# Performance work log

Hardware: AMD Instinct MI355X
Metric: run time of the kernel (lower is better)

Reference implementation:

```python
import jax, jax.numpy as jnp
import numpy as np

N = 100000   # nodes
E = 1600000  # edges (avg degree 16)
H = 128      # hidden_dim
G = 256      # graphs in batch
IN = 2       # input feature dim (GCNConv(2, hidden_dim))


def setup_inputs() -> dict:
    key = jax.random.key(0)
    ks = jax.random.split(key, 12)
    def lin(k, fan_in, shape):
        # kaiming-uniform-ish init, scale irrelevant for correctness testing
        return jax.random.uniform(k, shape, jnp.float32, -1.0, 1.0) / np.sqrt(fan_in).astype(np.float32)
    return {
        "x": jax.random.normal(ks[0], (N, IN), jnp.float32),
        "edge_src": jax.random.randint(ks[1], (E,), 0, N, jnp.int32),
        "edge_dst": jax.random.randint(ks[2], (E,), 0, N, jnp.int32),
        "batch_ids": jnp.sort(jax.random.randint(ks[3], (N,), 0, G, jnp.int32)),
        "num_graphs": G,
        "W1": lin(ks[4], IN, (IN, H)), "b1": jnp.zeros((H,), jnp.float32),
        "W2": lin(ks[5], H, (H, H)),  "b2": jnp.zeros((H,), jnp.float32),
        "fc1_W": lin(ks[6], H, (H, H)), "fc1_b": lin(ks[7], H, (H,)),
        "fc2_W": lin(ks[8], H, (H, 1)), "fc2_b": lin(ks[9], H, (1,)),
    }


def gcn_layer(x, W, b, src, dst, n):
    # PyG GCNConv: add self-loops, symmetric deg^{-1/2} normalization,
    # linear transform, scatter-add aggregation, bias.
    h = x @ W                                                     # [N, H]
    deg = jax.ops.segment_sum(jnp.ones_like(src, jnp.float32), dst, num_segments=n) + 1.0  # +1 self-loop
    dinv = jax.lax.rsqrt(deg)                                     # [N]
    norm = dinv[src] * dinv[dst]                                  # [E]
    agg = jax.ops.segment_sum(h[src] * norm[:, None], dst, num_segments=n)  # [N, H]
    # self-loop contribution: deg_i^{-1/2} * deg_i^{-1/2} = 1/deg_i
    return agg + h * (1.0 / deg)[:, None] + b


def reference(x, edge_src, edge_dst, batch_ids, num_graphs,
              W1, b1, W2, b2, fc1_W, fc1_b, fc2_W, fc2_b):
    n = x.shape[0]
    h = jax.nn.relu(gcn_layer(x, W1, b1, edge_src, edge_dst, n))
    h = jax.nn.relu(gcn_layer(h, W2, b2, edge_src, edge_dst, n))
    # global_mean_pool
    sums = jax.ops.segment_sum(h, batch_ids, num_segments=num_graphs)            # [G, H]
    cnt = jax.ops.segment_sum(jnp.ones((n,), jnp.float32), batch_ids, num_segments=num_graphs)
    pooled = sums / jnp.maximum(cnt, 1.0)[:, None]
    h = jax.nn.relu(pooled @ fc1_W + fc1_b)
    return h @ fc2_W + fc2_b                                                     # [G, 1]
```

## Files before the change

### kernel.cpp

```cpp
#include <hip/hip_runtime.h>
#include <stdint.h>

#define HD 128
#define BSH 8
#define BNODES 256
#define PER 8
#define SCAP 256
#define BINBLK 256

typedef float f32x4 __attribute__((ext_vector_type(4)));
typedef float f32x2 __attribute__((ext_vector_type(2)));
typedef short s16x8 __attribute__((ext_vector_type(8)));

static inline int idiv(int a, int b) { return (a + b - 1) / b; }

__device__ __forceinline__ unsigned short f2b(float f) {
  unsigned u = __float_as_uint(f);
  return (unsigned short)((u + 0x7fffu + ((u >> 16) & 1u)) >> 16);
}

__global__ void __launch_bounds__(256) k_bincount(const int* __restrict__ edst,
                                                  int* __restrict__ cntm,
                                                  int E, int NB, int chunk) {
  __shared__ int hist[512];
  int blk = blockIdx.x;
  for (int b = threadIdx.x; b < 512; b += 256) hist[b] = 0;
  __syncthreads();
  int s0 = blk * chunk, s1 = min(E, s0 + chunk);
  for (int k = s0 + threadIdx.x; k < s1; k += 256)
    atomicAdd(&hist[edst[k] >> BSH], 1);
  __syncthreads();
  for (int b = threadIdx.x; b < NB; b += 256)
    cntm[(size_t)b * BINBLK + blk] = hist[b];
}

__global__ void k_scan1(const int* __restrict__ cnt, int* __restrict__ part, int N) {
  __shared__ int sh[256];
  int t = threadIdx.x;
  int base = blockIdx.x * 1024 + t * 4;
  int s = 0;
#pragma unroll
  for (int u = 0; u < 4; ++u) { int idx = base + u; if (idx < N) s += cnt[idx]; }
  sh[t] = s; __syncthreads();
  for (int off = 128; off > 0; off >>= 1) { if (t < off) sh[t] += sh[t + off]; __syncthreads(); }
  if (t == 0) part[blockIdx.x] = sh[0];
}

__global__ void k_scan2(int* part, int nb) {
  __shared__ int sh[1024];
  int t = threadIdx.x;
  int v = (t < nb) ? part[t] : 0;
  sh[t] = v;
  __syncthreads();
  for (int off = 1; off < 1024; off <<= 1) {
    int add = (t >= off) ? sh[t - off] : 0;
    __syncthreads();
    sh[t] += add;
    __syncthreads();
  }
  if (t < nb) part[t] = sh[t] - v;
}

__global__ void k_scan3(const int* __restrict__ cnt, const int* __restrict__ part,
                        int* __restrict__ out, int N) {
  __shared__ int sa[256], sb[256];
  int t = threadIdx.x;
  int base = blockIdx.x * 1024 + t * 4;
  int v[4]; int s = 0;
#pragma unroll
  for (int u = 0; u < 4; ++u) { int idx = base + u; v[u] = (idx < N) ? cnt[idx] : 0; s += v[u]; }
  sa[t] = s; __syncthreads();
  int* cur = sa; int* nxt = sb;
  for (int off = 1; off < 256; off <<= 1) {
    int val = cur[t] + ((t >= off) ? cur[t - off] : 0);
    nxt[t] = val; __syncthreads();
    int* tmp = cur; cur = nxt; nxt = tmp;
  }
  int excl = cur[t] - s + part[blockIdx.x];
#pragma unroll
  for (int u = 0; u < 4; ++u) {
    int idx = base + u;
    if (idx < N) { out[idx] = excl; excl += v[u]; }
  }
}

__global__ void __launch_bounds__(256) k_binscatter(const int* __restrict__ esrc,
                                                    const int* __restrict__ edst,
                                                    const int* __restrict__ scanM,
                                                    unsigned* __restrict__ recs,
                                                    int E, int NB, int chunk) {
  __shared__ int cur[512];
  int blk = blockIdx.x;
  for (int b = threadIdx.x; b < NB; b += 256) cur[b] = scanM[(size_t)b * BINBLK + blk];
  __syncthreads();
  int s0 = blk * chunk, s1 = min(E, s0 + chunk);
  for (int k = s0 + threadIdx.x; k < s1; k += 256) {
    int d = edst[k], s = esrc[k];
    int b = d >> BSH;
    int pos = atomicAdd(&cur[b], 1);
    recs[pos] = ((unsigned)(d & (BNODES - 1)) << 23) | (unsigned)s;
  }
}

__global__ void __launch_bounds__(256) k_bucketsort(const unsigned* __restrict__ recs,
                                                    const int* __restrict__ scanM,
                                                    const float* __restrict__ x,
                                                    const int* __restrict__ bids,
                                                    unsigned* __restrict__ ssrc16,
                                                    int* __restrict__ row_start,
                                                    int* __restrict__ cnt,
                                                    float* __restrict__ dinv,
                                                    float2* __restrict__ xs,
                                                    int* __restrict__ gstart,
                                                    int NB, int N, int G, int E) {
  __shared__ int count[BNODES], excl[BNODES], cur[BNODES], psum[32];
  int b = blockIdx.x;
  int t = threadIdx.x;
  count[t] = 0;
  __syncthreads();
  int rs = scanM[(size_t)b * BINBLK];
  int re = (b == NB - 1) ? E : scanM[(size_t)(b + 1) * BINBLK];
  int base_p = rs + b * BNODES;
  for (int k = rs + t; k < re; k += 256) atomicAdd(&count[recs[k] >> 23], 1);
  __syncthreads();
  if (t < 32) {
    int s = 0;
#pragma unroll
    for (int u = 0; u < 8; ++u) s += (count[t * 8 + u] + 1) & ~1;
    psum[t] = s;
  }
  __syncthreads();
  if (t == 0) {
    int run = 0;
    for (int d = 0; d < 32; ++d) { int v = psum[d]; psum[d] = run; run += v; }
  }
  __syncthreads();
  if (t < 32) {
    int run = psum[t];
#pragma unroll
    for (int u = 0; u < 8; ++u) {
      excl[t * 8 + u] = run;
      run += (count[t * 8 + u] + 1) & ~1;
    }
  }
  __syncthreads();
  {
    int d = t;
    int i = b * BNODES + d;
    if (i < N) {
      cnt[i] = count[d];
      row_start[i] = base_p + excl[d];
      if (count[d] & 1)
        ssrc16[base_p + excl[d] + count[d]] = (unsigned)N << 4;
      float di = rsqrtf((float)(count[d] + 1));
      dinv[i] = di;
      float2 xv = *(const float2*)&x[2 * i];
      xs[i] = make_float2(di * xv.x, di * xv.y);
      int g = bids[i];
      if (i == 0)
        for (int gg = 0; gg <= g; ++gg) gstart[gg] = 0;
      int gn = (i == N - 1) ? G : bids[i + 1];
      for (int gg = g + 1; gg <= gn; ++gg) gstart[gg] = i + 1;
    }
    cur[d] = excl[d];
  }
  __syncthreads();
  for (int k = rs + t; k < re; k += 256) {
    unsigned r = recs[k];
    int dl = r >> 23;
    int pos = base_p + atomicAdd(&cur[dl], 1);
    ssrc16[pos] = (r & 0x007fffffu) << 4;
  }
}

__global__ void k_aggx2(const int* __restrict__ row_start, const int* __restrict__ cnt,
                        const unsigned* __restrict__ ssrc16, const float2* __restrict__ xs,
                        const float* __restrict__ dinv, float4* __restrict__ td, int N) {
  int i = blockIdx.x * 256 + threadIdx.x;
  if (i >= N) return;
  int rs = row_start[i], re = rs + cnt[i];
  float a0 = 0.f, a1 = 0.f, b0 = 0.f, b1 = 0.f;
  int k = rs;
  for (; k + 3 < re; k += 4) {
    unsigned v0 = ssrc16[k] >> 4, v1 = ssrc16[k + 1] >> 4;
    unsigned v2 = ssrc16[k + 2] >> 4, v3 = ssrc16[k + 3] >> 4;
    float2 p0 = xs[v0], p1 = xs[v1], p2 = xs[v2], p3 = xs[v3];
    a0 += p0.x + p1.x; a1 += p0.y + p1.y;
    b0 += p2.x + p3.x; b1 += p2.y + p3.y;
  }
  for (; k < re; ++k) {
    float2 p = xs[ssrc16[k] >> 4];
    a0 += p.x; a1 += p.y;
  }
  a0 += b0; a1 += b1;
  float2 self = xs[i];
  float di = dinv[i];
  td[i] = make_float4(di * (a0 + self.x), di * (a1 + self.y), di, 0.f);
}

__global__ void __launch_bounds__(256) k_aggh(
    const int* __restrict__ row_start, const int* __restrict__ cnt,
    const unsigned* __restrict__ ssrc16, const float4* __restrict__ td,
    const float* __restrict__ W1, const float* __restrict__ b1,
    unsigned* __restrict__ m_b, int N) {
  __shared__ float4 sbuf[4][SCAP];
  int wave = threadIdx.x >> 6;
  int lane = threadIdx.x & 63;
  int wid = blockIdx.x * 4 + wave;
  int i0 = wid * PER;
  if (i0 >= N) return;
  int nn = min(N - i0, PER);
  int hl = lane >> 5;
  int fq = (lane & 31) * 4;
  f32x4 w0 = *(const f32x4*)&W1[fq];
  f32x4 w1 = *(const f32x4*)&W1[HD + fq];
  f32x4 bb = *(const f32x4*)&b1[fq];
  int mydeg = (lane < nn) ? cnt[i0 + lane] : 0;
  int myrow = (lane < nn) ? row_start[i0 + lane] : 0;
  float4 mytd = (lane < nn) ? td[i0 + lane] : make_float4(0.f, 0.f, 0.f, 0.f);
  int mx = __float_as_int(mytd.x), my = __float_as_int(mytd.y), mz = __float_as_int(mytd.z);
  int rs0 = __builtin_amdgcn_readfirstlane(myrow);
  int last = nn - 1;
  int rsEnd = __builtin_amdgcn_readlane(myrow, last) +
              ((__builtin_amdgcn_readlane(mydeg, last) + 1) & ~1);
  int total = rsEnd - rs0;
  const char* tdc = (const char*)td;
  bool staged = (total <= SCAP);
  if (staged) {
#pragma unroll
    for (int w = 0; w < SCAP / 64; ++w) {
      int sl = w * 64 + lane;
      if (sl < total) {
        unsigned off = ssrc16[rs0 + sl];
        sbuf[wave][sl] = *(const float4*)(tdc + off);
      }
    }
  }
  int k = 0;
  const f32x4 zero4 = {0.f, 0.f, 0.f, 0.f};
#define EDGE_F(T, ACC) { \
    f32x4 h = f32x4{T.y, T.y, T.y, T.y} * w1 + bb; \
    h = f32x4{T.x, T.x, T.x, T.x} * w0 + h; \
    h = __builtin_elementwise_max(h, zero4); \
    ACC = f32x4{T.z, T.z, T.z, T.z} * h + ACC; }
  for (int node = 0; node < nn; ++node) {
    int deg = __builtin_amdgcn_readlane(mydeg, node);
    int np = (deg + 1) >> 1;
    f32x4 acc = zero4, acc2 = zero4;
    if (staged) {
      const float4* buf = &sbuf[wave][k + hl];
      int p = 0;
      for (; p + 1 < np; p += 2) {
        float4 t0 = buf[2 * p];
        float4 t1 = buf[2 * p + 2];
        EDGE_F(t0, acc)
        EDGE_F(t1, acc2)
      }
      if (p < np) {
        float4 t0 = buf[2 * p];
        EDGE_F(t0, acc)
      }
    } else {
      for (int p = 0; p < np; ++p) {
        unsigned off = ssrc16[rs0 + k + 2 * p + hl];
        float4 t = *(const float4*)(tdc + off);
        EDGE_F(t, acc)
      }
    }
    k += np * 2;
#pragma unroll
    for (int c = 0; c < 4; ++c) acc[c] += acc2[c];
    f32x4 tot;
#pragma unroll
    for (int c = 0; c < 4; ++c) tot[c] = acc[c] + __shfl_xor(acc[c], 32);
    float tx = __int_as_float(__builtin_amdgcn_readlane(mx, node));
    float ty = __int_as_float(__builtin_amdgcn_readlane(my, node));
    float tz = __int_as_float(__builtin_amdgcn_readlane(mz, node));
    f32x4 h = f32x4{ty, ty, ty, ty} * w1 + bb;
    h = f32x4{tx, tx, tx, tx} * w0 + h;
    h = __builtin_elementwise_max(h, zero4);
    f32x4 r = f32x4{tz, tz, tz, tz} * h + tot;
    float v0 = (hl ? r[2] : r[0]) * tz;
    float v1 = (hl ? r[3] : r[1]) * tz;
    int j = hl ? (2 * (lane - 32) + 1) : (2 * lane);
    m_b[(unsigned)(i0 + node) * 64 + j] = ((unsigned)f2b(v1) << 16) | f2b(v0);
  }
#undef EDGE_F
}

__global__ void k_w2t(const float* __restrict__ W2, unsigned* __restrict__ w2f,
                      float4* __restrict__ td, int N) {
  int f = blockIdx.x * 256 + threadIdx.x;
  if (f == 0) td[N] = make_float4(0.f, 0.f, 0.f, 0.f);
  if (f >= 2048) return;
  int c = f >> 8, s = (f >> 6) & 3, lane = f & 63;
  int col = c * 16 + (lane & 15);
  int kb = s * 32 + (lane >> 4) * 8;
  unsigned hi4[4], lo4[4];
#pragma unroll
  for (int j = 0; j < 4; ++j) {
    float w0 = W2[(kb + 2 * j) * HD + col];
    float w1 = W2[(kb + 2 * j + 1) * HD + col];
    unsigned short h0 = f2b(w0), h1 = f2b(w1);
    float r0 = w0 - __uint_as_float((unsigned)h0 << 16);
    float r1 = w1 - __uint_as_float((unsigned)h1 << 16);
    unsigned short l0 = f2b(r0), l1 = f2b(r1);
    hi4[j] = ((unsigned)h1 << 16) | h0;
    lo4[j] = ((unsigned)l1 << 16) | l0;
  }
  *(uint4*)&w2f[f * 4] = make_uint4(hi4[0], hi4[1], hi4[2], hi4[3]);
  *(uint4*)&w2f[8192 + f * 4] = make_uint4(lo4[0], lo4[1], lo4[2], lo4[3]);
}

__global__ void __launch_bounds__(256) k_t2pool(
    const unsigned* __restrict__ m_b, const unsigned* __restrict__ w2f,
    const float* __restrict__ b2, const int* __restrict__ gstart,
    const float* __restrict__ fc1W, const float* __restrict__ fc1b,
    const float* __restrict__ fc2W, const float* __restrict__ fc2b,
    float* __restrict__ out, int N, int G) {
  __shared__ unsigned W[16384];
  __shared__ float pool[16][HD];
  __shared__ float ps[HD];
  __shared__ float rsh[HD];
  int g = blockIdx.x;
  for (int u = threadIdx.x; u < 4096; u += 256)
    *(uint4*)&W[u * 4] = *(const uint4*)&w2f[u * 4];
  for (int u = threadIdx.x; u < 16 * HD; u += 256) ((float*)pool)[u] = 0.f;
  const int lane = threadIdx.x & 63;
  const int wave = threadIdx.x >> 6;
  const int col = lane & 15;
  const int kg = lane >> 4;
  float bb[8];
#pragma unroll
  for (int c = 0; c < 8; ++c) bb[c] = b2[c * 16 + col];
  int s0 = gstart[g], e0 = gstart[g + 1];
  int ntiles = (e0 - s0 + 15) >> 4;
  float pacc[8];
#pragma unroll
  for (int c = 0; c < 8; ++c) pacc[c] = 0.f;
  __syncthreads();
  for (int tile = wave; tile < ntiles; tile += 4) {
    int rbase = s0 + tile * 16;
    int arow = rbase + col;
    if (arow >= N) arow = N - 1;
    f32x4 acc[8];
#pragma unroll
    for (int c = 0; c < 8; ++c) acc[c] = f32x4{0.f, 0.f, 0.f, 0.f};
#pragma unroll
    for (int s = 0; s < 4; ++s) {
      uint4 av = *(const uint4*)&m_b[((size_t)arow << 6) + s * 16 + kg * 4];
      s16x8 A = *(s16x8*)&av;
#pragma unroll
      for (int c = 0; c < 8; ++c) {
        int f = (c * 4 + s) * 64 + lane;
        s16x8 Bh = *(s16x8*)&W[f * 4];
        s16x8 Bl = *(s16x8*)&W[8192 + f * 4];
        acc[c] = __builtin_amdgcn_mfma_f32_16x16x32_bf16(A, Bh, acc[c], 0, 0, 0);
        acc[c] = __builtin_amdgcn_mfma_f32_16x16x32_bf16(A, Bl, acc[c], 0, 0, 0);
      }
    }
    int orow = rbase + kg * 4;
#pragma unroll
    for (int c = 0; c < 8; ++c) {
#pragma unroll
      for (int r = 0; r < 4; ++r) {
        if (orow + r < e0) pacc[c] += fmaxf(acc[c][r] + bb[c], 0.f);
      }
    }
  }
#pragma unroll
  for (int c = 0; c < 8; ++c) pool[wave * 4 + kg][c * 16 + col] = pacc[c];
  __syncthreads();
  int j = threadIdx.x;
  if (j < HD) {
    float a = 0.f;
#pragma unroll
    for (int r = 0; r < 16; ++r) a += pool[r][j];
    float cg = (float)(e0 - s0);
    cg = cg < 1.f ? 1.f : cg;
    ps[j] = a / cg;
  }
  __syncthreads();
  if (j < HD) {
    float a = fc1b[j];
#pragma unroll 4
    for (int k = 0; k < HD; ++k) a = fmaf(ps[k], fc1W[k * HD + j], a);
    rsh[j] = fmaxf(a, 0.f) * fc2W[j];
  }
  __syncthreads();
  for (int off = 64; off > 0; off >>= 1) {
    if (j < off) rsh[j] += rsh[j + off];
    __syncthreads();
  }
  if (j == 0) out[g] = rsh[0] + fc2b[0];
}

extern "C" void kernel_launch(void* const* d_in, const int* in_sizes, int n_in,
                              void* d_out, int out_size, void* d_ws, size_t ws_size,
                              hipStream_t stream) {
  const float* x    = (const float*)d_in[0];
  const int* esrc   = (const int*)d_in[1];
  const int* edst   = (const int*)d_in[2];
  const int* bids   = (const int*)d_in[3];
  const float* W1   = (const float*)d_in[5];
  const float* b1   = (const float*)d_in[6];
  const float* W2   = (const float*)d_in[7];
  const float* b2   = (const float*)d_in[8];
  const float* fc1W = (const float*)d_in[9];
  const float* fc1b = (const float*)d_in[10];
  const float* fc2W = (const float*)d_in[11];
  const float* fc2b = (const float*)d_in[12];
  float* out = (float*)d_out;

  const int N = in_sizes[0] / 2;
  const int E = in_sizes[1];
  const int G = out_size;

  const int NB = idiv(N, BNODES);
  const int M = NB * BINBLK;
  const int chunk = idiv(E, BINBLK);

  char* w = (char*)d_ws;
  size_t o = 0;
  auto take = [&](size_t b) -> char* {
    char* p = w + o;
    o = (o + b + 255) & ~(size_t)255;
    return p;
  };
  int*      cntm      = (int*)     take((size_t)M * 4);
  int*      scanM     = (int*)     take((size_t)M * 4);
  int*      part      = (int*)     take(4096);
  unsigned* recs      = (unsigned*)take((size_t)E * 4);
  unsigned* ssrc16    = (unsigned*)take((size_t)(E + N + 256) * 4);
  int*      cnt       = (int*)     take((size_t)N * 4);
  int*      row_start = (int*)     take((size_t)N * 4);
  float*    dinv      = (float*)   take((size_t)N * 4);
  float*    xs        = (float*)   take((size_t)N * 8);
  float*    td        = (float*)   take((size_t)(N + 1) * 16);
  int*      gstart    = (int*)     take((size_t)(G + 1) * 4);
  unsigned* m_b       = (unsigned*)take((size_t)N * 64 * 4);
  unsigned* w2f       = (unsigned*)take(16384 * 4);

  int nbM = idiv(M, 1024);
  k_w2t<<<8, 256, 0, stream>>>(W2, w2f, (float4*)td, N);
  k_bincount<<<BINBLK, 256, 0, stream>>>(edst, cntm, E, NB, chunk);
  k_scan1<<<nbM, 256, 0, stream>>>(cntm, part, M);
  k_scan2<<<1, 1024, 0, stream>>>(part, nbM);
  k_scan3<<<nbM, 256, 0, stream>>>(cntm, part, scanM, M);
  k_binscatter<<<BINBLK, 256, 0, stream>>>(esrc, edst, scanM, recs, E, NB, chunk);
  k_bucketsort<<<NB, 256, 0, stream>>>(recs, scanM, x, bids, ssrc16, row_start,
                                       cnt, dinv, (float2*)xs, gstart, NB, N, G, E);
  k_aggx2<<<idiv(N, 256), 256, 0, stream>>>(row_start, cnt, ssrc16, (const float2*)xs,
                                            dinv, (float4*)td, N);
  int waves = idiv(N, PER);
  k_aggh<<<idiv(waves, 4), 256, 0, stream>>>(row_start, cnt, ssrc16, (const float4*)td,
                                             W1, b1, m_b, N);
  k_t2pool<<<G, 256, 0, stream>>>(m_b, w2f, b2, gstart, fc1W, fc1b, fc2W, fc2b, out, N, G);
}
```

Before: 126.0 us.

## Stream edge gathers through double-buffered LDS batches and merge scan kernels

The layer-2 aggregation kernel no longer stages a whole wave's edges in a fixed 256-entry LDS buffer with a slow uncached fallback. It now walks edges in 64-entry batches, double-buffered, prefetching the next batch into registers while computing the current one, with a per-node state machine that spans batch boundaries. Nodes per wave go from 8 to 16. The three-kernel scan over the bin-count matrix becomes a single 1024-thread kernel, cutting two launches at the cost of running on one block.

```diff
diff --git a/kernel.cpp b/kernel.cpp
--- a/kernel.cpp
+++ b/kernel.cpp
@@ -4,8 +4,7 @@
 #define HD 128
 #define BSH 8
 #define BNODES 256
-#define PER 8
-#define SCAP 256
+#define PER 16
 #define BINBLK 256
 
 typedef float f32x4 __attribute__((ext_vector_type(4)));
@@ -34,23 +33,18 @@
     cntm[(size_t)b * BINBLK + blk] = hist[b];
 }
 
-__global__ void k_scan1(const int* __restrict__ cnt, int* __restrict__ part, int N) {
-  __shared__ int sh[256];
-  int t = threadIdx.x;
-  int base = blockIdx.x * 1024 + t * 4;
-  int s = 0;
-#pragma unroll
-  for (int u = 0; u < 4; ++u) { int idx = base + u; if (idx < N) s += cnt[idx]; }
-  sh[t] = s; __syncthreads();
-  for (int off = 128; off > 0; off >>= 1) { if (t < off) sh[t] += sh[t + off]; __syncthreads(); }
-  if (t == 0) part[blockIdx.x] = sh[0];
-}
-
-__global__ void k_scan2(int* part, int nb) {
+__global__ void __launch_bounds__(1024) k_scanM(const int* __restrict__ cntm,
+                                                int* __restrict__ scanM, int M) {
   __shared__ int sh[1024];
   int t = threadIdx.x;
-  int v = (t < nb) ? part[t] : 0;
-  sh[t] = v;
+  int per = (M + 1023) >> 10;
+  int base = t * per;
+  int s = 0;
+  for (int u = 0; u < per; ++u) {
+    int idx = base + u;
+    if (idx < M) s += cntm[idx];
+  }
+  sh[t] = s;
   __syncthreads();
   for (int off = 1; off < 1024; off <<= 1) {
     int add = (t >= off) ? sh[t - off] : 0;
@@ -58,29 +52,14 @@
     sh[t] += add;
     __syncthreads();
   }
-  if (t < nb) part[t] = sh[t] - v;
-}
-
-__global__ void k_scan3(const int* __restrict__ cnt, const int* __restrict__ part,
-                        int* __restrict__ out, int N) {
-  __shared__ int sa[256], sb[256];
-  int t = threadIdx.x;
-  int base = blockIdx.x * 1024 + t * 4;
-  int v[4]; int s = 0;
-#pragma unroll
-  for (int u = 0; u < 4; ++u) { int idx = base + u; v[u] = (idx < N) ? cnt[idx] : 0; s += v[u]; }
-  sa[t] = s; __syncthreads();
-  int* cur = sa; int* nxt = sb;
-  for (int off = 1; off < 256; off <<= 1) {
-    int val = cur[t] + ((t >= off) ? cur[t - off] : 0);
-    nxt[t] = val; __syncthreads();
-    int* tmp = cur; cur = nxt; nxt = tmp;
-  }
-  int excl = cur[t] - s + part[blockIdx.x];
-#pragma unroll
-  for (int u = 0; u < 4; ++u) {
+  int excl = sh[t] - s;
+  for (int u = 0; u < per; ++u) {
     int idx = base + u;
-    if (idx < N) { out[idx] = excl; excl += v[u]; }
+    if (idx < M) {
+      int v = cntm[idx];
+      scanM[idx] = excl;
+      excl += v;
+    }
   }
 }
 
@@ -203,7 +182,7 @@
     const unsigned* __restrict__ ssrc16, const float4* __restrict__ td,
     const float* __restrict__ W1, const float* __restrict__ b1,
     unsigned* __restrict__ m_b, int N) {
-  __shared__ float4 sbuf[4][SCAP];
+  __shared__ float4 sbuf[4][2][64];
   int wave = threadIdx.x >> 6;
   int lane = threadIdx.x & 63;
   int wid = blockIdx.x * 4 + wave;
@@ -224,55 +203,26 @@
   int rsEnd = __builtin_amdgcn_readlane(myrow, last) +
               ((__builtin_amdgcn_readlane(mydeg, last) + 1) & ~1);
   int total = rsEnd - rs0;
+  int nbatch = (total + 63) >> 6;
   const char* tdc = (const char*)td;
-  bool staged = (total <= SCAP);
-  if (staged) {
-#pragma unroll
-    for (int w = 0; w < SCAP / 64; ++w) {
-      int sl = w * 64 + lane;
-      if (sl < total) {
-        unsigned off = ssrc16[rs0 + sl];
-        sbuf[wave][sl] = *(const float4*)(tdc + off);
-      }
-    }
-  }
-  int k = 0;
   const f32x4 zero4 = {0.f, 0.f, 0.f, 0.f};
 #define EDGE_F(T, ACC) { \
     f32x4 h = f32x4{T.y, T.y, T.y, T.y} * w1 + bb; \
     h = f32x4{T.x, T.x, T.x, T.x} * w0 + h; \
     h = __builtin_elementwise_max(h, zero4); \
     ACC = f32x4{T.z, T.z, T.z, T.z} * h + ACC; }
-  for (int node = 0; node < nn; ++node) {
-    int deg = __builtin_amdgcn_readlane(mydeg, node);
-    int np = (deg + 1) >> 1;
-    f32x4 acc = zero4, acc2 = zero4;
-    if (staged) {
-      const float4* buf = &sbuf[wave][k + hl];
-      int p = 0;
-      for (; p + 1 < np; p += 2) {
-        float4 t0 = buf[2 * p];
-        float4 t1 = buf[2 * p + 2];
-        EDGE_F(t0, acc)
-        EDGE_F(t1, acc2)
-      }
-      if (p < np) {
-        float4 t0 = buf[2 * p];
-        EDGE_F(t0, acc)
-      }
-    } else {
-      for (int p = 0; p < np; ++p) {
-        unsigned off = ssrc16[rs0 + k + 2 * p + hl];
-        float4 t = *(const float4*)(tdc + off);
-        EDGE_F(t, acc)
-      }
-    }
-    k += np * 2;
-#pragma unroll
-    for (int c = 0; c < 4; ++c) acc[c] += acc2[c];
+
+  int node = 0;
+  int remP = (__builtin_amdgcn_readlane(mydeg, 0) + 1) >> 1;
+  f32x4 acc = zero4, acc2 = zero4;
+
+  auto finishNode = [&]() {
     f32x4 tot;
 #pragma unroll
-    for (int c = 0; c < 4; ++c) tot[c] = acc[c] + __shfl_xor(acc[c], 32);
+    for (int c = 0; c < 4; ++c) {
+      float a = acc[c] + acc2[c];
+      tot[c] = a + __shfl_xor(a, 32);
+    }
     float tx = __int_as_float(__builtin_amdgcn_readlane(mx, node));
     float ty = __int_as_float(__builtin_amdgcn_readlane(my, node));
     float tz = __int_as_float(__builtin_amdgcn_readlane(mz, node));
@@ -284,7 +234,47 @@
     float v1 = (hl ? r[3] : r[1]) * tz;
     int j = hl ? (2 * (lane - 32) + 1) : (2 * lane);
     m_b[(unsigned)(i0 + node) * 64 + j] = ((unsigned)f2b(v1) << 16) | f2b(v0);
-  }
+    acc = zero4; acc2 = zero4;
+    ++node;
+    remP = (node < nn) ? ((__builtin_amdgcn_readlane(mydeg, node) + 1) >> 1)
+                       : 0x40000000;
+  };
+
+  if (nbatch) {
+    unsigned off = (lane < total) ? ssrc16[rs0 + lane] : 0u;
+    sbuf[wave][0][lane] = *(const float4*)(tdc + off);
+  }
+  for (int b = 0; b < nbatch; ++b) {
+    bool more = (b + 1 < nbatch);
+    float4 pre = make_float4(0.f, 0.f, 0.f, 0.f);
+    if (more) {
+      int sl = (b + 1) * 64 + lane;
+      unsigned off = (sl < total) ? ssrc16[rs0 + sl] : 0u;
+      pre = *(const float4*)(tdc + off);
+    }
+    int cp = min(64, total - b * 64) >> 1;
+    const float4* buf = &sbuf[wave][b & 1][hl];
+    int p = 0;
+    while (p < cp) {
+      while (remP == 0) finishNode();
+      int take = min(remP, cp - p);
+      int e = 0;
+      for (; e + 1 < take; e += 2) {
+        float4 t0 = buf[2 * (p + e)];
+        float4 t1 = buf[2 * (p + e) + 2];
+        EDGE_F(t0, acc)
+        EDGE_F(t1, acc2)
+      }
+      if (e < take) {
+        float4 t0 = buf[2 * (p + e)];
+        EDGE_F(t0, acc)
+      }
+      p += take;
+      remP -= take;
+    }
+    if (more) sbuf[wave][(b + 1) & 1][lane] = pre;
+  }
+  while (node < nn) finishNode();
 #undef EDGE_F
 }
 
@@ -429,7 +419,6 @@
   };
   int*      cntm      = (int*)     take((size_t)M * 4);
   int*      scanM     = (int*)     take((size_t)M * 4);
-  int*      part      = (int*)     take(4096);
   unsigned* recs      = (unsigned*)take((size_t)E * 4);
   unsigned* ssrc16    = (unsigned*)take((size_t)(E + N + 256) * 4);
   int*      cnt       = (int*)     take((size_t)N * 4);
@@ -441,12 +430,9 @@
   unsigned* m_b       = (unsigned*)take((size_t)N * 64 * 4);
   unsigned* w2f       = (unsigned*)take(16384 * 4);
 
-  int nbM = idiv(M, 1024);
   k_w2t<<<8, 256, 0, stream>>>(W2, w2f, (float4*)td, N);
   k_bincount<<<BINBLK, 256, 0, stream>>>(edst, cntm, E, NB, chunk);
-  k_scan1<<<nbM, 256, 0, stream>>>(cntm, part, M);
-  k_scan2<<<1, 1024, 0, stream>>>(part, nbM);
-  k_scan3<<<nbM, 256, 0, stream>>>(cntm, part, scanM, M);
+  k_scanM<<<1, 1024, 0, stream>>>(cntm, scanM, M);
   k_binscatter<<<BINBLK, 256, 0, stream>>>(esrc, edst, scanM, recs, E, NB, chunk);
   k_bucketsort<<<NB, 256, 0, stream>>>(recs, scanM, x, bids, ssrc16, row_start,
                                        cnt, dinv, (float2*)xs, gstart, NB, N, G, E);
```

After: 312.9 us. 148% more time.
